# Performance work log

Measured on AMD Instinct MI355X. Metric: run time of the kernel, lower is better.

## Reference

```python
import jax, jax.numpy as jnp
import numpy as np

N_NODES = 100000
N_EDGES = 3200000
IN_DIM, HID_DIM, OUT_DIM = 768, 50, 2


def gcn_conv(x, W, b, row, col, deg_isqrt, n_nodes):
    # PyG GCNConv: h = x @ W, then symmetric-normalized scatter-add (self-loops
    # already included in row/col), then + bias.
    h = x @ W                                    # [N, out]
    norm = deg_isqrt[row] * deg_isqrt[col]       # [E+N]
    msgs = h[row] * norm[:, None]                # gather + scale
    out = jax.ops.segment_sum(msgs, col, num_segments=n_nodes)
    return out + b


def _augment(edge_index, n_nodes):
    # add self-loops and compute D^{-1/2} with self-loops
    loops = jnp.arange(n_nodes, dtype=edge_index.dtype)
    row = jnp.concatenate([edge_index[0], loops])
    col = jnp.concatenate([edge_index[1], loops])
    deg = jax.ops.segment_sum(jnp.ones_like(col, dtype=jnp.float32), col,
                              num_segments=n_nodes)
    deg_isqrt = jnp.where(deg > 0, jax.lax.rsqrt(deg), 0.0)
    return row, col, deg_isqrt


def setup_inputs() -> dict:
    key = jax.random.key(0)
    k1, k2, k3, k4 = jax.random.split(key, 4)
    x = jax.random.normal(k1, (N_NODES, IN_DIM), dtype=jnp.float32)
    edge_index = jax.random.randint(k2, (2, N_EDGES), 0, N_NODES, dtype=jnp.int64)
    W1 = jax.random.normal(k3, (IN_DIM, HID_DIM), dtype=jnp.float32) / np.sqrt(IN_DIM)
    b1 = jnp.zeros((HID_DIM,), dtype=jnp.float32)
    W2 = jax.random.normal(k4, (HID_DIM, OUT_DIM), dtype=jnp.float32) / np.sqrt(HID_DIM)
    b2 = jnp.zeros((OUT_DIM,), dtype=jnp.float32)
    return {"x": x, "edge_index": edge_index, "W1": W1, "b1": b1, "W2": W2, "b2": b2}


def reference(x, edge_index, W1, b1, W2, b2):
    n = x.shape[0]
    row, col, deg_isqrt = _augment(edge_index, n)
    h = gcn_conv(x, W1, b1, row, col, deg_isqrt, n)   # GCNConv(768 -> 50)
    h = jax.nn.relu(h)                                 # ReLU
    h = gcn_conv(h, W2, b2, row, col, deg_isqrt, n)   # GCNConv(50 -> 2)
    return jax.nn.sigmoid(h)                           # Sigmoid output layer
```

## Files before the change

kernel.cpp:

```cpp
#include <hip/hip_runtime.h>


#define N_NODES 100000
#define N_EDGES 3200000
#define IN_DIM  768
#define HID     50
#define HIDP    52
#define SCAN_BLK 1024
#define NSCAN_BLKS 98
#define NPAD (NSCAN_BLKS * SCAN_BLK)
#define NKSTEP (IN_DIM / 32)

using s8v = __attribute__((ext_vector_type(8))) short;
using f4v = __attribute__((ext_vector_type(4))) float;

__device__ __forceinline__ short f2bf(float f) {
  union { float f; unsigned u; } v; v.f = f;
  unsigned r = (v.u + 0x7fffu + ((v.u >> 16) & 1u)) >> 16;
  return (short)r;
}
__device__ __forceinline__ float bf2f(unsigned short u) {
  union { unsigned u; float f; } v; v.u = ((unsigned)u) << 16;
  return v.f;
}


__global__ void k_count(const int* __restrict__ edges, int* __restrict__ cnt) {
  int e = blockIdx.x * 256 + threadIdx.x;
  if (e < N_EDGES) atomicAdd(&cnt[edges[N_EDGES + e]], 1);
}

__global__ void k_scanA(const int* __restrict__ cnt, int* __restrict__ offs,
                        int* __restrict__ bsum) {
  __shared__ int s[SCAN_BLK];
  int t = threadIdx.x;
  int g = blockIdx.x * SCAN_BLK + t;
  int v = (g < N_NODES) ? cnt[g] : 0;
  s[t] = v;
  __syncthreads();
  for (int off = 1; off < SCAN_BLK; off <<= 1) {
    int add = (t >= off) ? s[t - off] : 0;
    __syncthreads();
    s[t] += add;
    __syncthreads();
  }
  offs[g] = s[t] - v;
  if (t == SCAN_BLK - 1) bsum[blockIdx.x] = s[t];
}

__global__ void k_scanB(int* __restrict__ bsum) {
  __shared__ int s[128];
  int t = threadIdx.x;
  int v = (t < NSCAN_BLKS) ? bsum[t] : 0;
  s[t] = v;
  __syncthreads();
  for (int off = 1; off < 128; off <<= 1) {
    int add = (t >= off) ? s[t - off] : 0;
    __syncthreads();
    s[t] += add;
    __syncthreads();
  }
  if (t < NSCAN_BLKS) bsum[t] = s[t] - v;
}

__global__ void k_scanC(int* __restrict__ cnt, int* __restrict__ offs,
                        const int* __restrict__ bsum, float* __restrict__ dis) {
  int g = blockIdx.x * 256 + threadIdx.x;
  if (g < NPAD) {
    offs[g] += bsum[g >> 10];
    if (g < N_NODES) {
      dis[g] = rsqrtf((float)cnt[g] + 1.0f);
      cnt[g] = 0;
    }
  }
}

__global__ void k_fill(const int* __restrict__ edges, int* __restrict__ cnt,
                       const int* __restrict__ offs, int* __restrict__ eidx) {
  int e = blockIdx.x * 256 + threadIdx.x;
  if (e < N_EDGES) {
    int r = edges[e];
    int c = edges[N_EDGES + e];
    int p = atomicAdd(&cnt[c], 1);
    eidx[offs[c] + p] = r;
  }
}


__global__ void k_wprep(const float* __restrict__ W1, short* __restrict__ Bfrag) {
  int g = blockIdx.x * 256 + threadIdx.x;
  int s = g >> 8, r = g & 255;
  int nt = r >> 6, l = r & 63;
  int col = l & 15, quad = l >> 4;
  int n = nt * 16 + col;
  int kb = s * 32 + quad * 8;
  s8v o;
#pragma unroll
  for (int j = 0; j < 8; ++j)
    o[j] = (n < HID) ? f2bf(W1[(size_t)(kb + j) * HID + n]) : (short)0;
  *(s8v*)(Bfrag + (size_t)g * 8) = o;
}


__global__ __launch_bounds__(256) void k_gemm1(const float* __restrict__ x,
                                               const short* __restrict__ Bfrag,
                                               const float* __restrict__ dis,
                                               unsigned short* __restrict__ h1) {
  int t = threadIdx.x;
  int wave = t >> 6, lane = t & 63;
  int col = lane & 15, quad = lane >> 4;
  int rb = blockIdx.x * 64 + wave * 16;
  int arow = rb + col;
  if (arow > N_NODES - 1) arow = N_NODES - 1;
  const float* xrow = x + (size_t)arow * IN_DIM + quad * 8;
  const short* bbase = Bfrag + (size_t)lane * 8;

  f4v acc[4] = {f4v{0.f,0.f,0.f,0.f}, f4v{0.f,0.f,0.f,0.f},
                f4v{0.f,0.f,0.f,0.f}, f4v{0.f,0.f,0.f,0.f}};

#pragma unroll
  for (int s = 0; s < NKSTEP; ++s) {
    float4 va = *(const float4*)(xrow + s * 32);
    float4 vb = *(const float4*)(xrow + s * 32 + 4);
    s8v b0 = *(const s8v*)(bbase + (size_t)(s * 4 + 0) * 512);
    s8v b1 = *(const s8v*)(bbase + (size_t)(s * 4 + 1) * 512);
    s8v b2 = *(const s8v*)(bbase + (size_t)(s * 4 + 2) * 512);
    s8v b3 = *(const s8v*)(bbase + (size_t)(s * 4 + 3) * 512);
    s8v a;
    a[0] = f2bf(va.x); a[1] = f2bf(va.y); a[2] = f2bf(va.z); a[3] = f2bf(va.w);
    a[4] = f2bf(vb.x); a[5] = f2bf(vb.y); a[6] = f2bf(vb.z); a[7] = f2bf(vb.w);
    acc[0] = __builtin_amdgcn_mfma_f32_16x16x32_bf16(a, b0, acc[0], 0, 0, 0);
    acc[1] = __builtin_amdgcn_mfma_f32_16x16x32_bf16(a, b1, acc[1], 0, 0, 0);
    acc[2] = __builtin_amdgcn_mfma_f32_16x16x32_bf16(a, b2, acc[2], 0, 0, 0);
    acc[3] = __builtin_amdgcn_mfma_f32_16x16x32_bf16(a, b3, acc[3], 0, 0, 0);
  }

  int node0 = rb + quad * 4;
  float dd[4];
#pragma unroll
  for (int r = 0; r < 4; ++r)
    dd[r] = (node0 + r < N_NODES) ? dis[node0 + r] : 0.f;
#pragma unroll
  for (int nt = 0; nt < 4; ++nt) {
    int c = nt * 16 + col;
    if (c < HIDP) {
#pragma unroll
      for (int r = 0; r < 4; ++r) {
        int node = node0 + r;
        if (node < N_NODES)
          h1[(size_t)node * HIDP + c] = (unsigned short)f2bf(acc[nt][r] * dd[r]);
      }
    }
  }
}


__global__ __launch_bounds__(256) void k_agg1(
    const unsigned short* __restrict__ h1, const int* __restrict__ eidx,
    const int* __restrict__ offs, const float* __restrict__ dis,
    const float* __restrict__ b1, const float* __restrict__ W2,
    float* __restrict__ h2s) {
  __shared__ float W2s[2][64];
  __shared__ float b1s[64];
  int t = threadIdx.x;
  if (t < 64) {
    b1s[t] = (t < HID) ? b1[t] : 0.f;
    W2s[0][t] = (t < HID) ? W2[t * 2 + 0] : 0.f;
    W2s[1][t] = (t < HID) ? W2[t * 2 + 1] : 0.f;
  }
  __syncthreads();
  int wave = t >> 6, lane = t & 63;
  int n = blockIdx.x * 4 + wave;
  if (n >= N_NODES) return;
  int way = lane >> 4, L = lane & 15;
  int base = L * 4;
  bool actC = base < HIDP;
  int baseS = actC ? base : 0;
  int start = offs[n];
  int end = (n == N_NODES - 1) ? N_EDGES : offs[n + 1];

  float a0 = 0.f, a1 = 0.f, a2 = 0.f, a3 = 0.f;
  int i  = start + way;
  int idx  = (i  < end) ? eidx[i]  : n;
  ushort4 u = *(const ushort4*)(h1 + (size_t)idx * HIDP + baseS);
  int i2 = i + 4;
  int idx2 = (i2 < end) ? eidx[i2] : n;
  while (i < end) {
    ushort4 u2 = *(const ushort4*)(h1 + (size_t)idx2 * HIDP + baseS);
    int i3 = i2 + 4;
    int idx3 = (i3 < end) ? eidx[i3] : n;
    a0 += bf2f(u.x); a1 += bf2f(u.y); a2 += bf2f(u.z); a3 += bf2f(u.w);
    u = u2; idx2 = idx3; i = i2; i2 = i3;
  }

  a0 += __shfl_xor(a0, 16); a0 += __shfl_xor(a0, 32);
  a1 += __shfl_xor(a1, 16); a1 += __shfl_xor(a1, 32);
  a2 += __shfl_xor(a2, 16); a2 += __shfl_xor(a2, 32);
  a3 += __shfl_xor(a3, 16); a3 += __shfl_xor(a3, 32);

  float p0 = 0.f, p1 = 0.f;
  if (actC && way == 0) {
    float dn = dis[n];
    ushort4 us = *(const ushort4*)(h1 + (size_t)n * HIDP + base);
    float s0 = (a0 + bf2f(us.x)) * dn + b1s[base + 0];
    float s1 = (a1 + bf2f(us.y)) * dn + b1s[base + 1];
    float s2 = (a2 + bf2f(us.z)) * dn + b1s[base + 2];
    float s3 = (a3 + bf2f(us.w)) * dn + b1s[base + 3];
    s0 = fmaxf(s0, 0.f); s1 = fmaxf(s1, 0.f);
    s2 = fmaxf(s2, 0.f); s3 = fmaxf(s3, 0.f);
    p0 = s0 * W2s[0][base] + s1 * W2s[0][base + 1] +
         s2 * W2s[0][base + 2] + s3 * W2s[0][base + 3];
    p1 = s0 * W2s[1][base] + s1 * W2s[1][base + 1] +
         s2 * W2s[1][base + 2] + s3 * W2s[1][base + 3];
  }
  for (int m = 8; m; m >>= 1) {
    p0 += __shfl_xor(p0, m, 16);
    p1 += __shfl_xor(p1, m, 16);
  }
  if (lane == 0) {
    float dn = dis[n];
    h2s[(size_t)n * 2 + 0] = p0 * dn;
    h2s[(size_t)n * 2 + 1] = p1 * dn;
  }
}


__global__ __launch_bounds__(256) void k_agg2(
    const float* __restrict__ h2s, const int* __restrict__ eidx,
    const int* __restrict__ offs, const float* __restrict__ dis,
    const float* __restrict__ b2, float* __restrict__ out) {
  int t = threadIdx.x;
  int wave = t >> 6, lane = t & 63;
  int n = blockIdx.x * 4 + wave;
  if (n >= N_NODES) return;
  int start = offs[n];
  int end = (n == N_NODES - 1) ? N_EDGES : offs[n + 1];
  float s0 = 0.f, s1 = 0.f;
  for (int i = start + lane; i < end; i += 64) {
    int idx = eidx[i];
    float2 v = *(const float2*)(h2s + (size_t)idx * 2);
    s0 += v.x; s1 += v.y;
  }
  for (int m = 32; m; m >>= 1) {
    s0 += __shfl_xor(s0, m);
    s1 += __shfl_xor(s1, m);
  }
  if (lane == 0) {
    float dn = dis[n];
    float2 v = *(const float2*)(h2s + (size_t)n * 2);
    float r0 = (s0 + v.x) * dn + b2[0];
    float r1 = (s1 + v.y) * dn + b2[1];
    out[(size_t)n * 2 + 0] = 1.f / (1.f + __expf(-r0));
    out[(size_t)n * 2 + 1] = 1.f / (1.f + __expf(-r1));
  }
}


static inline size_t aln(size_t v) { return (v + 255) & ~(size_t)255; }

extern "C" void kernel_launch(void* const* d_in, const int* in_sizes, int n_in,
                              void* d_out, int out_size, void* d_ws, size_t ws_size,
                              hipStream_t stream) {
  const float* x     = (const float*)d_in[0];
  const int*   edges = (const int*)d_in[1];
  const float* W1    = (const float*)d_in[2];
  const float* b1    = (const float*)d_in[3];
  const float* W2    = (const float*)d_in[4];
  const float* b2    = (const float*)d_in[5];
  float* out = (float*)d_out;

  char* p = (char*)d_ws;
  int* cnt  = (int*)p;            p += aln((size_t)NPAD * 4);
  int* offs = (int*)p;            p += aln((size_t)NPAD * 4);
  int* bsum = (int*)p;            p += aln((size_t)NSCAN_BLKS * 4);
  float* dis = (float*)p;         p += aln((size_t)N_NODES * 4);
  int* eidx = (int*)p;            p += aln((size_t)N_EDGES * 4);
  short* Bfrag = (short*)p;       p += aln((size_t)NKSTEP * 4 * 64 * 8 * 2);
  unsigned short* h1 = (unsigned short*)p; p += aln((size_t)N_NODES * HIDP * 2);
  float* h2s = (float*)p;         p += aln((size_t)N_NODES * 2 * 4);

  int gN   = (NPAD + 255) / 256;
  int gE   = (N_EDGES + 255) / 256;
  int gMM  = (N_NODES + 63) / 64;
  int gW   = (N_NODES + 3) / 4;

  hipMemsetAsync(cnt, 0, (size_t)NPAD * 4, stream);
  k_count<<<gE, 256, 0, stream>>>(edges, cnt);
  k_scanA<<<NSCAN_BLKS, SCAN_BLK, 0, stream>>>(cnt, offs, bsum);
  k_scanB<<<1, 128, 0, stream>>>(bsum);
  k_scanC<<<gN, 256, 0, stream>>>(cnt, offs, bsum, dis);
  k_fill <<<gE, 256, 0, stream>>>(edges, cnt, offs, eidx);
  k_wprep<<<NKSTEP, 256, 0, stream>>>(W1, Bfrag);
  k_gemm1<<<gMM, 256, 0, stream>>>(x, Bfrag, dis, h1);
  k_agg1 <<<gW, 256, 0, stream>>>(h1, eidx, offs, dis, b1, W2, h2s);
  k_agg2 <<<gW, 256, 0, stream>>>(h2s, eidx, offs, dis, b2, out);
}
```

Baseline: 839.2 us.

## Fuse CSR build stages, merge fill with GEMM, double-buffer and widen GEMM tiles

The count kernel now records each edge's atomic slot so the fill pass needs no second atomic. The three scan kernels and the weight prep collapse into one launch that uses a decoupled block-prefix via spin-waiting on flags. Edge fill runs in the same launch as the GEMM so the two overlap. The GEMM handles 32 rows per wave with register double-buffering and a cheaper packed bf16 conversion. h1 rows are padded to 64 elements for shift indexing, and nontemporal loads are added. Risks include a spin-wait deadlock if scan blocks are not co-resident, and changed rounding behaviour.

```diff
diff --git a/kernel.cpp b/kernel.cpp
--- a/kernel.cpp
+++ b/kernel.cpp
@@ -5,19 +5,34 @@
 #define N_EDGES 3200000
 #define IN_DIM  768
 #define HID     50
-#define HIDP    52
+#define HIDP    64
+#define HWID    52
 #define SCAN_BLK 1024
 #define NSCAN_BLKS 98
 #define NPAD (NSCAN_BLKS * SCAN_BLK)
-#define NKSTEP (IN_DIM / 32)
+#define NKSTEP 24
+#define GEMM_BLOCKS 782
+#define FILL_BLOCKS 3125
+#define WPREP_BLOCKS 6
 
 using s8v = __attribute__((ext_vector_type(8))) short;
-using f4v = __attribute__((ext_vector_type(4))) float;
-
-__device__ __forceinline__ short f2bf(float f) {
+using f4  = __attribute__((ext_vector_type(4))) float;
+using u4  = __attribute__((ext_vector_type(4))) unsigned;
+using i4  = __attribute__((ext_vector_type(4))) int;
+
+__device__ __forceinline__ unsigned pkbf(unsigned lo, unsigned hi) {
+  return __builtin_amdgcn_perm(hi + 0x8000u, lo + 0x8000u, 0x07060302);
+}
+__device__ __forceinline__ s8v cvt8(f4 a, f4 b) {
+  u4 ua = __builtin_bit_cast(u4, a), ub = __builtin_bit_cast(u4, b);
+  u4 r;
+  r[0] = pkbf(ua[0], ua[1]); r[1] = pkbf(ua[2], ua[3]);
+  r[2] = pkbf(ub[0], ub[1]); r[3] = pkbf(ub[2], ub[3]);
+  return __builtin_bit_cast(s8v, r);
+}
+__device__ __forceinline__ unsigned short f2bf_u(float f) {
   union { float f; unsigned u; } v; v.f = f;
-  unsigned r = (v.u + 0x7fffu + ((v.u >> 16) & 1u)) >> 16;
-  return (short)r;
+  return (unsigned short)((v.u + 0x8000u) >> 16);
 }
 __device__ __forceinline__ float bf2f(unsigned short u) {
   union { unsigned u; float f; } v; v.u = ((unsigned)u) << 16;
@@ -25,16 +40,44 @@
 }
 
 
-__global__ void k_count(const int* __restrict__ edges, int* __restrict__ cnt) {
-  int e = blockIdx.x * 256 + threadIdx.x;
-  if (e < N_EDGES) atomicAdd(&cnt[edges[N_EDGES + e]], 1);
-}
-
-__global__ void k_scanA(const int* __restrict__ cnt, int* __restrict__ offs,
-                        int* __restrict__ bsum) {
+__global__ __launch_bounds__(256) void k_count(const int* __restrict__ edges,
+                                               int* __restrict__ cnt,
+                                               int* __restrict__ pos) {
+  int e0 = (blockIdx.x * 256 + threadIdx.x) * 4;
+  i4 c = __builtin_nontemporal_load((const i4*)(edges + N_EDGES + e0));
+  i4 p;
+  p[0] = atomicAdd(&cnt[c[0]], 1);
+  p[1] = atomicAdd(&cnt[c[1]], 1);
+  p[2] = atomicAdd(&cnt[c[2]], 1);
+  p[3] = atomicAdd(&cnt[c[3]], 1);
+  __builtin_nontemporal_store(p, (i4*)(pos + e0));
+}
+
+
+__global__ __launch_bounds__(1024) void k_scan(
+    const int* __restrict__ cnt, int* __restrict__ offs,
+    float* __restrict__ dis, int* __restrict__ bsum,
+    const float* __restrict__ W1, short* __restrict__ Bfrag) {
+  int b = blockIdx.x;
+  int t = threadIdx.x;
+  if (b >= NSCAN_BLKS) {
+    int g = (b - NSCAN_BLKS) * 1024 + t;
+    int s = g >> 8, r = g & 255;
+    int ct = r >> 6, l = r & 63;
+    int n = ct * 16 + (l & 15);
+    int kb = s * 32 + (l >> 4) * 8;
+    s8v o;
+#pragma unroll
+    for (int j = 0; j < 8; ++j) {
+      float w = (n < HID) ? W1[(size_t)(kb + j) * HID + n] : 0.f;
+      o[j] = (short)f2bf_u(w);
+    }
+    *(s8v*)(Bfrag + (size_t)g * 8) = o;
+    return;
+  }
   __shared__ int s[SCAN_BLK];
-  int t = threadIdx.x;
-  int g = blockIdx.x * SCAN_BLK + t;
+  __shared__ int stot[128];
+  int g = b * SCAN_BLK + t;
   int v = (g < N_NODES) ? cnt[g] : 0;
   s[t] = v;
   __syncthreads();
@@ -44,111 +87,107 @@
     s[t] += add;
     __syncthreads();
   }
-  offs[g] = s[t] - v;
-  if (t == SCAN_BLK - 1) bsum[blockIdx.x] = s[t];
-}
-
-__global__ void k_scanB(int* __restrict__ bsum) {
-  __shared__ int s[128];
-  int t = threadIdx.x;
-  int v = (t < NSCAN_BLKS) ? bsum[t] : 0;
-  s[t] = v;
+  if (t == SCAN_BLK - 1)
+    __hip_atomic_store(&bsum[b], s[t], __ATOMIC_RELEASE, __HIP_MEMORY_SCOPE_AGENT);
+  if (t < 128) {
+    int pv = 0;
+    if (t < b) {
+      do {
+        pv = __hip_atomic_load(&bsum[t], __ATOMIC_ACQUIRE, __HIP_MEMORY_SCOPE_AGENT);
+      } while (pv == -1);
+    }
+    stot[t] = pv;
+  }
+  for (int o = 64; o; o >>= 1) {
+    __syncthreads();
+    if (t < o) stot[t] += stot[t + o];
+  }
   __syncthreads();
-  for (int off = 1; off < 128; off <<= 1) {
-    int add = (t >= off) ? s[t - off] : 0;
-    __syncthreads();
-    s[t] += add;
-    __syncthreads();
-  }
-  if (t < NSCAN_BLKS) bsum[t] = s[t] - v;
-}
-
-__global__ void k_scanC(int* __restrict__ cnt, int* __restrict__ offs,
-                        const int* __restrict__ bsum, float* __restrict__ dis) {
-  int g = blockIdx.x * 256 + threadIdx.x;
-  if (g < NPAD) {
-    offs[g] += bsum[g >> 10];
-    if (g < N_NODES) {
-      dis[g] = rsqrtf((float)cnt[g] + 1.0f);
-      cnt[g] = 0;
-    }
-  }
-}
-
-__global__ void k_fill(const int* __restrict__ edges, int* __restrict__ cnt,
-                       const int* __restrict__ offs, int* __restrict__ eidx) {
-  int e = blockIdx.x * 256 + threadIdx.x;
-  if (e < N_EDGES) {
-    int r = edges[e];
-    int c = edges[N_EDGES + e];
-    int p = atomicAdd(&cnt[c], 1);
-    eidx[offs[c] + p] = r;
-  }
-}
-
-
-__global__ void k_wprep(const float* __restrict__ W1, short* __restrict__ Bfrag) {
-  int g = blockIdx.x * 256 + threadIdx.x;
-  int s = g >> 8, r = g & 255;
-  int nt = r >> 6, l = r & 63;
-  int col = l & 15, quad = l >> 4;
-  int n = nt * 16 + col;
-  int kb = s * 32 + quad * 8;
-  s8v o;
-#pragma unroll
-  for (int j = 0; j < 8; ++j)
-    o[j] = (n < HID) ? f2bf(W1[(size_t)(kb + j) * HID + n]) : (short)0;
-  *(s8v*)(Bfrag + (size_t)g * 8) = o;
-}
-
-
-__global__ __launch_bounds__(256) void k_gemm1(const float* __restrict__ x,
-                                               const short* __restrict__ Bfrag,
-                                               const float* __restrict__ dis,
-                                               unsigned short* __restrict__ h1) {
+  int prefix = stot[0];
+  offs[g] = prefix + s[t] - v;
+  if (g < N_NODES) dis[g] = rsqrtf((float)cnt[g] + 1.0f);
+}
+
+
+__global__ __launch_bounds__(256) void k_fillgemm(
+    const float* __restrict__ x, const short* __restrict__ Bfrag,
+    const float* __restrict__ dis, unsigned short* __restrict__ h1,
+    const int* __restrict__ edges, const int* __restrict__ pos,
+    const int* __restrict__ offs, int* __restrict__ eidx) {
+  if (blockIdx.x >= GEMM_BLOCKS) {
+    int e0 = ((blockIdx.x - GEMM_BLOCKS) * 256 + threadIdx.x) * 4;
+    i4 r = __builtin_nontemporal_load((const i4*)(edges + e0));
+    i4 c = __builtin_nontemporal_load((const i4*)(edges + N_EDGES + e0));
+    i4 p = __builtin_nontemporal_load((const i4*)(pos + e0));
+    eidx[offs[c[0]] + p[0]] = r[0];
+    eidx[offs[c[1]] + p[1]] = r[1];
+    eidx[offs[c[2]] + p[2]] = r[2];
+    eidx[offs[c[3]] + p[3]] = r[3];
+    return;
+  }
   int t = threadIdx.x;
   int wave = t >> 6, lane = t & 63;
   int col = lane & 15, quad = lane >> 4;
-  int rb = blockIdx.x * 64 + wave * 16;
-  int arow = rb + col;
-  if (arow > N_NODES - 1) arow = N_NODES - 1;
-  const float* xrow = x + (size_t)arow * IN_DIM + quad * 8;
-  const short* bbase = Bfrag + (size_t)lane * 8;
-
-  f4v acc[4] = {f4v{0.f,0.f,0.f,0.f}, f4v{0.f,0.f,0.f,0.f},
-                f4v{0.f,0.f,0.f,0.f}, f4v{0.f,0.f,0.f,0.f}};
+  int rb = blockIdx.x * 128 + wave * 32;
+  int ar0 = rb + col;       if (ar0 > N_NODES - 1) ar0 = N_NODES - 1;
+  int ar1 = rb + 16 + col;  if (ar1 > N_NODES - 1) ar1 = N_NODES - 1;
+  const float* xr0 = x + (size_t)ar0 * IN_DIM + quad * 8;
+  const float* xr1 = x + (size_t)ar1 * IN_DIM + quad * 8;
+  const short* bb = Bfrag + (size_t)lane * 8;
+
+  f4 A[2][4]; s8v B[2][4];
+  f4 acc[8] = {};
+
+  A[0][0] = __builtin_nontemporal_load((const f4*)(xr0));
+  A[0][1] = __builtin_nontemporal_load((const f4*)(xr0 + 4));
+  A[0][2] = __builtin_nontemporal_load((const f4*)(xr1));
+  A[0][3] = __builtin_nontemporal_load((const f4*)(xr1 + 4));
+#pragma unroll
+  for (int j = 0; j < 4; ++j) B[0][j] = *(const s8v*)(bb + (size_t)j * 512);
 
 #pragma unroll
   for (int s = 0; s < NKSTEP; ++s) {
-    float4 va = *(const float4*)(xrow + s * 32);
-    float4 vb = *(const float4*)(xrow + s * 32 + 4);
-    s8v b0 = *(const s8v*)(bbase + (size_t)(s * 4 + 0) * 512);
-    s8v b1 = *(const s8v*)(bbase + (size_t)(s * 4 + 1) * 512);
-    s8v b2 = *(const s8v*)(bbase + (size_t)(s * 4 + 2) * 512);
-    s8v b3 = *(const s8v*)(bbase + (size_t)(s * 4 + 3) * 512);
-    s8v a;
-    a[0] = f2bf(va.x); a[1] = f2bf(va.y); a[2] = f2bf(va.z); a[3] = f2bf(va.w);
-    a[4] = f2bf(vb.x); a[5] = f2bf(vb.y); a[6] = f2bf(vb.z); a[7] = f2bf(vb.w);
-    acc[0] = __builtin_amdgcn_mfma_f32_16x16x32_bf16(a, b0, acc[0], 0, 0, 0);
-    acc[1] = __builtin_amdgcn_mfma_f32_16x16x32_bf16(a, b1, acc[1], 0, 0, 0);
-    acc[2] = __builtin_amdgcn_mfma_f32_16x16x32_bf16(a, b2, acc[2], 0, 0, 0);
-    acc[3] = __builtin_amdgcn_mfma_f32_16x16x32_bf16(a, b3, acc[3], 0, 0, 0);
-  }
-
-  int node0 = rb + quad * 4;
-  float dd[4];
-#pragma unroll
-  for (int r = 0; r < 4; ++r)
-    dd[r] = (node0 + r < N_NODES) ? dis[node0 + r] : 0.f;
-#pragma unroll
-  for (int nt = 0; nt < 4; ++nt) {
-    int c = nt * 16 + col;
-    if (c < HIDP) {
-#pragma unroll
-      for (int r = 0; r < 4; ++r) {
-        int node = node0 + r;
-        if (node < N_NODES)
-          h1[(size_t)node * HIDP + c] = (unsigned short)f2bf(acc[nt][r] * dd[r]);
+    int cur = s & 1, nxt = cur ^ 1;
+    if (s + 1 < NKSTEP) {
+      const float* p0 = xr0 + (s + 1) * 32;
+      const float* p1 = xr1 + (s + 1) * 32;
+      A[nxt][0] = __builtin_nontemporal_load((const f4*)p0);
+      A[nxt][1] = __builtin_nontemporal_load((const f4*)(p0 + 4));
+      A[nxt][2] = __builtin_nontemporal_load((const f4*)p1);
+      A[nxt][3] = __builtin_nontemporal_load((const f4*)(p1 + 4));
+#pragma unroll
+      for (int j = 0; j < 4; ++j)
+        B[nxt][j] = *(const s8v*)(bb + (size_t)((s + 1) * 4 + j) * 512);
+    }
+    s8v a0 = cvt8(A[cur][0], A[cur][1]);
+    s8v a1 = cvt8(A[cur][2], A[cur][3]);
+    acc[0] = __builtin_amdgcn_mfma_f32_16x16x32_bf16(a0, B[cur][0], acc[0], 0, 0, 0);
+    acc[1] = __builtin_amdgcn_mfma_f32_16x16x32_bf16(a0, B[cur][1], acc[1], 0, 0, 0);
+    acc[2] = __builtin_amdgcn_mfma_f32_16x16x32_bf16(a0, B[cur][2], acc[2], 0, 0, 0);
+    acc[3] = __builtin_amdgcn_mfma_f32_16x16x32_bf16(a0, B[cur][3], acc[3], 0, 0, 0);
+    acc[4] = __builtin_amdgcn_mfma_f32_16x16x32_bf16(a1, B[cur][0], acc[4], 0, 0, 0);
+    acc[5] = __builtin_amdgcn_mfma_f32_16x16x32_bf16(a1, B[cur][1], acc[5], 0, 0, 0);
+    acc[6] = __builtin_amdgcn_mfma_f32_16x16x32_bf16(a1, B[cur][2], acc[6], 0, 0, 0);
+    acc[7] = __builtin_amdgcn_mfma_f32_16x16x32_bf16(a1, B[cur][3], acc[7], 0, 0, 0);
+  }
+
+#pragma unroll
+  for (int half = 0; half < 2; ++half) {
+    int node0 = rb + half * 16 + quad * 4;
+    float dd[4];
+#pragma unroll
+    for (int r = 0; r < 4; ++r)
+      dd[r] = (node0 + r < N_NODES) ? dis[node0 + r] : 0.f;
+#pragma unroll
+    for (int ct = 0; ct < 4; ++ct) {
+      int c = ct * 16 + col;
+      if (c < HWID) {
+#pragma unroll
+        for (int r = 0; r < 4; ++r) {
+          int node = node0 + r;
+          if (node < N_NODES)
+            h1[((size_t)node << 6) + c] = f2bf_u(acc[half * 4 + ct][r] * dd[r]);
+        }
       }
     }
   }
@@ -174,21 +213,21 @@
   if (n >= N_NODES) return;
   int way = lane >> 4, L = lane & 15;
   int base = L * 4;
-  bool actC = base < HIDP;
+  bool actC = base < HWID;
   int baseS = actC ? base : 0;
   int start = offs[n];
-  int end = (n == N_NODES - 1) ? N_EDGES : offs[n + 1];
+  int end = offs[n + 1];
 
   float a0 = 0.f, a1 = 0.f, a2 = 0.f, a3 = 0.f;
   int i  = start + way;
-  int idx  = (i  < end) ? eidx[i]  : n;
-  ushort4 u = *(const ushort4*)(h1 + (size_t)idx * HIDP + baseS);
+  int idx  = (i  < end) ? __builtin_nontemporal_load(eidx + i)  : n;
+  ushort4 u = *(const ushort4*)(h1 + ((size_t)idx << 6) + baseS);
   int i2 = i + 4;
-  int idx2 = (i2 < end) ? eidx[i2] : n;
+  int idx2 = (i2 < end) ? __builtin_nontemporal_load(eidx + i2) : n;
   while (i < end) {
-    ushort4 u2 = *(const ushort4*)(h1 + (size_t)idx2 * HIDP + baseS);
+    ushort4 u2 = *(const ushort4*)(h1 + ((size_t)idx2 << 6) + baseS);
     int i3 = i2 + 4;
-    int idx3 = (i3 < end) ? eidx[i3] : n;
+    int idx3 = (i3 < end) ? __builtin_nontemporal_load(eidx + i3) : n;
     a0 += bf2f(u.x); a1 += bf2f(u.y); a2 += bf2f(u.z); a3 += bf2f(u.w);
     u = u2; idx2 = idx3; i = i2; i2 = i3;
   }
@@ -201,7 +240,7 @@
   float p0 = 0.f, p1 = 0.f;
   if (actC && way == 0) {
     float dn = dis[n];
-    ushort4 us = *(const ushort4*)(h1 + (size_t)n * HIDP + base);
+    ushort4 us = *(const ushort4*)(h1 + ((size_t)n << 6) + base);
     float s0 = (a0 + bf2f(us.x)) * dn + b1s[base + 0];
     float s1 = (a1 + bf2f(us.y)) * dn + b1s[base + 1];
     float s2 = (a2 + bf2f(us.z)) * dn + b1s[base + 2];
@@ -234,10 +273,10 @@
   int n = blockIdx.x * 4 + wave;
   if (n >= N_NODES) return;
   int start = offs[n];
-  int end = (n == N_NODES - 1) ? N_EDGES : offs[n + 1];
+  int end = offs[n + 1];
   float s0 = 0.f, s1 = 0.f;
   for (int i = start + lane; i < end; i += 64) {
-    int idx = eidx[i];
+    int idx = __builtin_nontemporal_load(eidx + i);
     float2 v = *(const float2*)(h2s + (size_t)idx * 2);
     s0 += v.x; s1 += v.y;
   }
@@ -272,26 +311,21 @@
   char* p = (char*)d_ws;
   int* cnt  = (int*)p;            p += aln((size_t)NPAD * 4);
   int* offs = (int*)p;            p += aln((size_t)NPAD * 4);
-  int* bsum = (int*)p;            p += aln((size_t)NSCAN_BLKS * 4);
+  int* bsum = (int*)p;            p += aln((size_t)128 * 4);
   float* dis = (float*)p;         p += aln((size_t)N_NODES * 4);
   int* eidx = (int*)p;            p += aln((size_t)N_EDGES * 4);
+  int* pos  = (int*)p;            p += aln((size_t)N_EDGES * 4);
   short* Bfrag = (short*)p;       p += aln((size_t)NKSTEP * 4 * 64 * 8 * 2);
   unsigned short* h1 = (unsigned short*)p; p += aln((size_t)N_NODES * HIDP * 2);
   float* h2s = (float*)p;         p += aln((size_t)N_NODES * 2 * 4);
 
-  int gN   = (NPAD + 255) / 256;
-  int gE   = (N_EDGES + 255) / 256;
-  int gMM  = (N_NODES + 63) / 64;
-  int gW   = (N_NODES + 3) / 4;
-
-  hipMemsetAsync(cnt, 0, (size_t)NPAD * 4, stream);
-  k_count<<<gE, 256, 0, stream>>>(edges, cnt);
-  k_scanA<<<NSCAN_BLKS, SCAN_BLK, 0, stream>>>(cnt, offs, bsum);
-  k_scanB<<<1, 128, 0, stream>>>(bsum);
-  k_scanC<<<gN, 256, 0, stream>>>(cnt, offs, bsum, dis);
-  k_fill <<<gE, 256, 0, stream>>>(edges, cnt, offs, eidx);
-  k_wprep<<<NKSTEP, 256, 0, stream>>>(W1, Bfrag);
-  k_gemm1<<<gMM, 256, 0, stream>>>(x, Bfrag, dis, h1);
-  k_agg1 <<<gW, 256, 0, stream>>>(h1, eidx, offs, dis, b1, W2, h2s);
-  k_agg2 <<<gW, 256, 0, stream>>>(h2s, eidx, offs, dis, b2, out);
-}
+  hipMemsetAsync(cnt, 0, (size_t)N_NODES * 4, stream);
+  hipMemsetAsync(bsum, 0xFF, (size_t)NSCAN_BLKS * 4, stream);
+  k_count<<<FILL_BLOCKS, 256, 0, stream>>>(edges, cnt, pos);
+  k_scan<<<NSCAN_BLKS + WPREP_BLOCKS, SCAN_BLK, 0, stream>>>(cnt, offs, dis,
+                                                             bsum, W1, Bfrag);
+  k_fillgemm<<<GEMM_BLOCKS + FILL_BLOCKS, 256, 0, stream>>>(x, Bfrag, dis, h1,
+                                                            edges, pos, offs, eidx);
+  k_agg1<<<(N_NODES + 3) / 4, 256, 0, stream>>>(h1, eidx, offs, dis, b1, W2, h2s);
+  k_agg2<<<(N_NODES + 3) / 4, 256, 0, stream>>>(h2s, eidx, offs, dis, b2, out);
+}
```

Result: faster. 789.7 us (-5.9%).
